# Kernel tuning notes

Hardware: AMD Instinct MI355X
Metric: run time of the kernel (lower is better)

Reference implementation:

```python
import jax, jax.numpy as jnp
import numpy as np
import math

D_MODEL = 1024
NHEAD = 16
FACTOR = 5


def setup_inputs() -> dict:
    key = jax.random.key(0)
    kq, kk, kv = jax.random.split(key, 3)
    B, L = 4, 2048
    Q = jax.random.normal(kq, (B, L, D_MODEL), dtype=jnp.float32)
    K = jax.random.normal(kk, (B, L, D_MODEL), dtype=jnp.float32)
    V = jax.random.normal(kv, (B, L, D_MODEL), dtype=jnp.float32)
    return {"Q": Q, "K": K, "V": V}


def reference(Q, K, V):
    B, q_len, _ = Q.shape
    k_len = K.shape[1]
    head_dim = D_MODEL // NHEAD
    scale = 1.0 / math.sqrt(head_dim)

    # [B, H, L, Dh]
    Qh = Q.reshape(B, q_len, NHEAD, head_dim).transpose(0, 2, 1, 3)
    Kh = K.reshape(B, k_len, NHEAD, head_dim).transpose(0, 2, 1, 3)
    Vh = V.reshape(B, k_len, NHEAD, head_dim).transpose(0, 2, 1, 3)

    # Dense scores for KL-based query selection
    scores = jnp.einsum('bhqd,bhkd->bhqk', Qh, Kh) * scale
    logp = jax.nn.log_softmax(scores, axis=-1)
    probs = jnp.exp(logp)
    # KL(p || uniform) = sum p * (log p + log k_len)
    kl_div = jnp.sum(probs * (logp + jnp.log(jnp.float32(k_len))), axis=-1)  # [B,H,Q]

    top_u = min(int(FACTOR * math.log(q_len)), q_len)
    _, indices = jax.lax.top_k(kl_div, top_u)  # [B,H,U]

    # Gather selected queries
    Q_sparse = jnp.take_along_axis(Qh, indices[..., None], axis=2)  # [B,H,U,Dh]
    scores_sparse = jnp.einsum('bhud,bhkd->bhuk', Q_sparse, Kh) * scale
    attn_weights = jax.nn.softmax(scores_sparse, axis=-1)  # dropout p=0 (eval)
    output_sparse = jnp.einsum('bhuk,bhkd->bhud', attn_weights, Vh)

    # Scatter back into full-length output (non-selected queries are zero)
    b_idx = jnp.arange(B)[:, None, None]
    h_idx = jnp.arange(NHEAD)[None, :, None]
    output_full = jnp.zeros_like(Qh).at[b_idx, h_idx, indices].set(output_sparse)

    output = output_full.transpose(0, 2, 1, 3).reshape(B, q_len, D_MODEL)
    return output, attn_weights
```

## Files before the change

### kernel.cpp

```cpp
#include <hip/hip_runtime.h>
#include <math.h>

#define LQ 2048
#define DM 1024
#define NH 16
#define DH 64
#define UU 38
#define NBH 64
#define SCALE 0.125f

typedef _Float16 f16x8 __attribute__((ext_vector_type(8)));
typedef float f32x4 __attribute__((ext_vector_type(4)));

#if __has_builtin(__builtin_amdgcn_exp2f)
#define EXP2F(x) __builtin_amdgcn_exp2f(x)
#else
#define EXP2F(x) exp2f(x)
#endif

#define F_OFF_SEL   4194304
#define F_OFF_L3    4204032
#define F_OFF_MASK  4213760
#define F_OFF_LPART 4344832
#define F_OFF_KSP   7146496
#define F_NEED      40700928ull

__global__ __launch_bounds__(256) void ksplit_kernel(const float* __restrict__ K,
                                                     _Float16* __restrict__ ksp) {
  int idx = blockIdx.x * 256 + threadIdx.x;
  int p = idx & 7;
  int k = (idx >> 3) & 63;
  int kc = (idx >> 9) & 31;
  int bh = idx >> 14;
  int b = bh >> 4, h = bh & 15;
  const float* src = K + ((size_t)(b * LQ + kc * 64 + k)) * DM + h * DH + (p ^ (k & 7)) * 8;
  float4 x0 = *(const float4*)src;
  float4 x1 = *(const float4*)(src + 4);
  f16x8 hi, lo;
#define KCV(i, xx) { float x_ = (xx); _Float16 hh = (_Float16)x_; hi[i] = hh; lo[i] = (_Float16)(x_ - (float)hh); }
  KCV(0, x0.x) KCV(1, x0.y) KCV(2, x0.z) KCV(3, x0.w)
  KCV(4, x1.x) KCV(5, x1.y) KCV(6, x1.z) KCV(7, x1.w)
#undef KCV
  _Float16* base = ksp + ((size_t)(bh * 32 + kc)) * 8192;
  *(f16x8*)(base + k * 64 + p * 8) = hi;
  *(f16x8*)(base + 4096 + k * 64 + p * 8) = lo;
}

__global__ __launch_bounds__(256) void kl_mfma2(const float* __restrict__ Q,
                                                const _Float16* __restrict__ ksp,
                                                double* __restrict__ lt) {
  int bh = blockIdx.x & 63;
  int qc = (blockIdx.x >> 6) & 15;
  int sp = blockIdx.x >> 10;
  int b = bh >> 4, h = bh & 15;
  int t = threadIdx.x;
  int lane = t & 63, w = t >> 6;
  int quad = lane >> 4, l15 = lane & 15;

  __shared__ __align__(16) _Float16 kbuf[8192];

  f16x8 ahi[2][2], alo[2][2];
  {
    const float* qrow = Q + ((size_t)(b * LQ + qc * 128)) * DM + h * DH;
#pragma unroll
    for (int qt = 0; qt < 2; ++qt)
#pragma unroll
      for (int c = 0; c < 2; ++c) {
        const float* p = qrow + (size_t)(w * 32 + qt * 16 + l15) * DM + c * 32 + quad * 8;
        float4 x0 = *(const float4*)p;
        float4 x1 = *(const float4*)(p + 4);
        f16x8 hi, lo;
#define QCV(i, xx) { float x_ = (xx); _Float16 hh = (_Float16)x_; hi[i] = hh; lo[i] = (_Float16)(x_ - (float)hh); }
        QCV(0, x0.x) QCV(1, x0.y) QCV(2, x0.z) QCV(3, x0.w)
        QCV(4, x1.x) QCV(5, x1.y) QCV(6, x1.z) QCV(7, x1.w)
#undef QCV
        ahi[qt][c] = hi;
        alo[qt][c] = lo;
      }
  }

  int bsw0 = quad ^ (l15 & 7);
  int bsw1 = (quad + 4) ^ (l15 & 7);
  _Float16* khi = kbuf;
  _Float16* klo = kbuf + 4096;
  const float C1 = 0.18033688011112042f;

  double l64[2][4], t64[2][4];
#pragma unroll
  for (int qt = 0; qt < 2; ++qt)
#pragma unroll
    for (int r = 0; r < 4; ++r) { l64[qt][r] = 0.0; t64[qt][r] = 0.0; }

  const uint4* gbase = (const uint4*)(ksp + ((size_t)(bh * 32 + sp * 16)) * 8192);
  uint4* lbuf = (uint4*)kbuf;

  for (int c = 0; c < 16; ++c) {
    const uint4* gsrc = gbase + (size_t)c * 1024;
    __syncthreads();
#pragma unroll
    for (int i = 0; i < 4; ++i) lbuf[i * 256 + t] = gsrc[i * 256 + t];
    __syncthreads();

    float l32[2][4], t32[2][4];
#pragma unroll
    for (int qt = 0; qt < 2; ++qt)
#pragma unroll
      for (int r = 0; r < 4; ++r) { l32[qt][r] = 0.f; t32[qt][r] = 0.f; }

#pragma unroll
    for (int kt = 0; kt < 4; ++kt) {
      int key = kt * 16 + l15;
      f16x8 bhi0 = *(const f16x8*)(khi + key * 64 + bsw0 * 8);
      f16x8 bhi1 = *(const f16x8*)(khi + key * 64 + bsw1 * 8);
      f16x8 blo0 = *(const f16x8*)(klo + key * 64 + bsw0 * 8);
      f16x8 blo1 = *(const f16x8*)(klo + key * 64 + bsw1 * 8);
#pragma unroll
      for (int qt = 0; qt < 2; ++qt) {
        f32x4 cacc = {0.f, 0.f, 0.f, 0.f};
        cacc = __builtin_amdgcn_mfma_f32_16x16x32_f16(alo[qt][0], bhi0, cacc, 0, 0, 0);
        cacc = __builtin_amdgcn_mfma_f32_16x16x32_f16(alo[qt][1], bhi1, cacc, 0, 0, 0);
        cacc = __builtin_amdgcn_mfma_f32_16x16x32_f16(ahi[qt][0], blo0, cacc, 0, 0, 0);
        cacc = __builtin_amdgcn_mfma_f32_16x16x32_f16(ahi[qt][1], blo1, cacc, 0, 0, 0);
        cacc = __builtin_amdgcn_mfma_f32_16x16x32_f16(ahi[qt][0], bhi0, cacc, 0, 0, 0);
        cacc = __builtin_amdgcn_mfma_f32_16x16x32_f16(ahi[qt][1], bhi1, cacc, 0, 0, 0);
#pragma unroll
        for (int r = 0; r < 4; ++r) {
          float rr = cacc[r];
          float e = EXP2F(rr * C1);
          l32[qt][r] += e;
          t32[qt][r] = fmaf(rr, e, t32[qt][r]);
        }
      }
    }
#pragma unroll
    for (int qt = 0; qt < 2; ++qt)
#pragma unroll
      for (int r = 0; r < 4; ++r) {
        l64[qt][r] += (double)l32[qt][r];
        t64[qt][r] += (double)t32[qt][r];
      }
  }

#pragma unroll
  for (int qt = 0; qt < 2; ++qt)
#pragma unroll
    for (int r = 0; r < 4; ++r) {
      double lv = l64[qt][r], tv = t64[qt][r];
#pragma unroll
      for (int m = 1; m < 16; m <<= 1) {
        lv += __shfl_xor(lv, m);
        tv += __shfl_xor(tv, m);
      }
      if (l15 == 0) {
        int qg = qc * 128 + w * 32 + qt * 16 + quad * 4 + r;
        double* dst = lt + ((size_t)(sp * 64 + bh) * LQ + qg) * 2;
        dst[0] = lv;
        dst[1] = tv;
      }
    }
}

__global__ __launch_bounds__(64) void topk2(const double* __restrict__ lt,
                                            int* __restrict__ idxout,
                                            signed char* __restrict__ selmask) {
  int bh = blockIdx.x;
  int lane = threadIdx.x;
  __shared__ double vals[LQ];
  const double logL = 7.624618986159398;
  double bv = -INFINITY;
  int bi = LQ;
  for (int j = 0; j < 32; ++j) {
    int i = j * 64 + lane;
    const double* p0 = lt + ((size_t)bh * LQ + i) * 2;
    const double* p1 = lt + ((size_t)(64 + bh) * LQ + i) * 2;
    double l = p0[0] + p1[0];
    double tt = p0[1] + p1[1];
    double v = 0.125 * (tt / l) - log(l) + logL;
    vals[i] = v;
    selmask[bh * LQ + i] = -1;
    if (v > bv) { bv = v; bi = i; }
  }
  for (int u = 0; u < UU; ++u) {
    double gv = bv;
    int gi = bi;
#pragma unroll
    for (int m = 1; m < 64; m <<= 1) {
      double ov = __shfl_xor(gv, m);
      int oi = __shfl_xor(gi, m);
      if (ov > gv || (ov == gv && oi < gi)) { gv = ov; gi = oi; }
    }
    if (lane == 0) {
      idxout[bh * UU + u] = gi;
      selmask[bh * LQ + gi] = (signed char)u;
    }
    if ((gi & 63) == lane) {
      vals[gi] = -INFINITY;
      bv = -INFINITY;
      bi = LQ;
      for (int j = 0; j < 32; ++j) {
        int i = j * 64 + lane;
        double v = vals[i];
        if (v > bv) { bv = v; bi = i; }
      }
    }
  }
}

__global__ __launch_bounds__(256) void attn_w_mfma(const float* __restrict__ Q,
                                                   const _Float16* __restrict__ ksp,
                                                   const int* __restrict__ sel,
                                                   float* __restrict__ wout,
                                                   float* __restrict__ lpart) {
  int bh = blockIdx.x >> 4;
  int ks = blockIdx.x & 15;
  int b = bh >> 4, h = bh & 15;
  int t = threadIdx.x;
  int lane = t & 63, w = t >> 6;
  int quad = lane >> 4, l15 = lane & 15;

  __shared__ __align__(16) _Float16 kbuf[8192];
  __shared__ float els[48 * 132];
  __shared__ int sidx[UU];

  if (t < UU) sidx[t] = sel[bh * UU + t];
  __syncthreads();

  f16x8 ahi[3][2], alo[3][2];
#pragma unroll
  for (int qt = 0; qt < 3; ++qt) {
    int u = qt * 16 + l15;
    if (u > 37) u = 37;
    const float* qrow = Q + ((size_t)(b * LQ + sidx[u])) * DM + h * DH;
#pragma unroll
    for (int c = 0; c < 2; ++c) {
      const float* p = qrow + c * 32 + quad * 8;
      float4 x0 = *(const float4*)p;
      float4 x1 = *(const float4*)(p + 4);
      f16x8 hi, lo;
#define QCV(i, xx) { float x_ = (xx); _Float16 hh = (_Float16)x_; hi[i] = hh; lo[i] = (_Float16)(x_ - (float)hh); }
      QCV(0, x0.x) QCV(1, x0.y) QCV(2, x0.z) QCV(3, x0.w)
      QCV(4, x1.x) QCV(5, x1.y) QCV(6, x1.z) QCV(7, x1.w)
#undef QCV
      ahi[qt][c] = hi;
      alo[qt][c] = lo;
    }
  }

  int bsw0 = quad ^ (l15 & 7);
  int bsw1 = (quad + 4) ^ (l15 & 7);
  const float C1 = 0.18033688011112042f;
  const uint4* gbase = (const uint4*)(ksp + ((size_t)(bh * 32 + ks * 2)) * 8192);
  uint4* lbuf = (uint4*)kbuf;
  _Float16* khi = kbuf;
  _Float16* klo = kbuf + 4096;

  for (int chunk = 0; chunk < 2; ++chunk) {
    __syncthreads();
#pragma unroll
    for (int i = 0; i < 4; ++i) lbuf[i * 256 + t] = gbase[chunk * 1024 + i * 256 + t];
    __syncthreads();
    int key = w * 16 + l15;
    f16x8 bhi0 = *(const f16x8*)(khi + key * 64 + bsw0 * 8);
    f16x8 bhi1 = *(const f16x8*)(khi + key * 64 + bsw1 * 8);
    f16x8 blo0 = *(const f16x8*)(klo + key * 64 + bsw0 * 8);
    f16x8 blo1 = *(const f16x8*)(klo + key * 64 + bsw1 * 8);
#pragma unroll
    for (int qt = 0; qt < 3; ++qt) {
      f32x4 cacc = {0.f, 0.f, 0.f, 0.f};
      cacc = __builtin_amdgcn_mfma_f32_16x16x32_f16(alo[qt][0], bhi0, cacc, 0, 0, 0);
      cacc = __builtin_amdgcn_mfma_f32_16x16x32_f16(alo[qt][1], bhi1, cacc, 0, 0, 0);
      cacc = __builtin_amdgcn_mfma_f32_16x16x32_f16(ahi[qt][0], blo0, cacc, 0, 0, 0);
      cacc = __builtin_amdgcn_mfma_f32_16x16x32_f16(ahi[qt][1], blo1, cacc, 0, 0, 0);
      cacc = __builtin_amdgcn_mfma_f32_16x16x32_f16(ahi[qt][0], bhi0, cacc, 0, 0, 0);
      cacc = __builtin_amdgcn_mfma_f32_16x16x32_f16(ahi[qt][1], bhi1, cacc, 0, 0, 0);
#pragma unroll
      for (int r = 0; r < 4; ++r) {
        float e = EXP2F(cacc[r] * C1);
        els[(qt * 16 + quad * 4 + r) * 132 + chunk * 64 + w * 16 + l15] = e;
      }
    }
  }
  __syncthreads();

  for (int i = t; i < UU * 128; i += 256) {
    int u = i >> 7, k = i & 127;
    wout[((size_t)(bh * UU + u)) * LQ + ks * 128 + k] = els[u * 132 + k];
  }

#pragma unroll
  for (int p = 0; p < 10; ++p) {
    int u = w + 4 * p;
    if (u < UU) {
      float s = els[u * 132 + lane] + els[u * 132 + 64 + lane];
#pragma unroll
      for (int m = 1; m < 64; m <<= 1) s += __shfl_xor(s, m);
      if (lane == 0) lpart[(bh * 16 + ks) * UU + u] = s;
    }
  }
}

__global__ __launch_bounds__(256) void attn_pv2(const float* __restrict__ V,
                                                const float* __restrict__ wout,
                                                const float* __restrict__ lpart,
                                                float* __restrict__ opart,
                                                float* __restrict__ l3) {
  int bh = blockIdx.x >> 4;
  int ks = blockIdx.x & 15;
  int b = bh >> 4, h = bh & 15;
  int t = threadIdx.x;
  int d = t & 63, ug = t >> 6;

  if (ks == 0 && t < UU) {
    float s = 0.f;
#pragma unroll
    for (int i = 0; i < 16; ++i) s += lpart[(bh * 16 + i) * UU + t];
    l3[bh * UU + t] = s;
  }

  __shared__ float ps[40 * 132];
  for (int i = t; i < UU * 32; i += 256) {
    int u = i >> 5, d4 = i & 31;
    *(float4*)(ps + u * 132 + d4 * 4) =
        *(const float4*)(wout + ((size_t)(bh * UU + u)) * LQ + ks * 128 + d4 * 4);
  }
  for (int i = t; i < 2 * 132; i += 256) ps[UU * 132 + i] = 0.f;
  __syncthreads();

  const float* vbase = V + ((size_t)(b * LQ + ks * 128)) * DM + h * DH + d;
  float o[10];
#pragma unroll
  for (int p = 0; p < 10; ++p) o[p] = 0.f;

  for (int j4 = 0; j4 < 128; j4 += 4) {
    float v0 = vbase[(size_t)(j4 + 0) * DM];
    float v1 = vbase[(size_t)(j4 + 1) * DM];
    float v2 = vbase[(size_t)(j4 + 2) * DM];
    float v3 = vbase[(size_t)(j4 + 3) * DM];
#pragma unroll
    for (int p = 0; p < 10; ++p) {
      float4 pw = *(const float4*)(ps + (ug + 4 * p) * 132 + j4);
      o[p] = fmaf(pw.x, v0, o[p]);
      o[p] = fmaf(pw.y, v1, o[p]);
      o[p] = fmaf(pw.z, v2, o[p]);
      o[p] = fmaf(pw.w, v3, o[p]);
    }
  }

#pragma unroll
  for (int p = 0; p < 10; ++p) {
    int u = ug + 4 * p;
    if (u < UU) opart[((size_t)((bh * 16 + ks) * UU + u)) * DH + d] = o[p];
  }
}

__global__ __launch_bounds__(256) void writeout_kernel(const signed char* __restrict__ selmask,
                                                       const float* __restrict__ l3,
                                                       const float* __restrict__ opart,
                                                       float* __restrict__ out,
                                                       float* __restrict__ wout) {
  const int N1 = NBH * UU * LQ;
  int i = blockIdx.x * 256 + threadIdx.x;
  if (i < N1) {
    wout[i] = wout[i] / l3[i >> 11];
  } else {
    int i2 = i - N1;
    int d = i2 & 63;
    int h = (i2 >> 6) & 15;
    int q = (i2 >> 10) & 2047;
    int b = i2 >> 21;
    int bh = b * 16 + h;
    int u = selmask[bh * LQ + q];
    float val = 0.f;
    if (u >= 0) {
      float s = 0.f;
#pragma unroll
      for (int p = 0; p < 16; ++p)
        s += opart[((size_t)((bh * 16 + p) * UU + u)) * DH + d];
      val = s / l3[bh * UU + u];
    }
    out[i2] = val;
  }
}

extern "C" void kernel_launch(void* const* d_in, const int* in_sizes, int n_in,
                              void* d_out, int out_size, void* d_ws, size_t ws_size,
                              hipStream_t stream) {
  (void)in_sizes; (void)n_in;
  if (ws_size < F_NEED) return;
  const float* Q = (const float*)d_in[0];
  const float* K = (const float*)d_in[1];
  const float* V = (const float*)d_in[2];
  float* out = (float*)d_out;
  float* wout = out + (size_t)4 * LQ * DM;
  char* ws = (char*)d_ws;

  double* lt = (double*)ws;
  int* sel = (int*)(ws + F_OFF_SEL);
  float* l3 = (float*)(ws + F_OFF_L3);
  signed char* mask = (signed char*)(ws + F_OFF_MASK);
  float* lpart = (float*)(ws + F_OFF_LPART);
  _Float16* ksp = (_Float16*)(ws + F_OFF_KSP);
  float* opart = (float*)(ws + F_OFF_KSP);

  ksplit_kernel<<<4096, 256, 0, stream>>>(K, ksp);
  kl_mfma2<<<2048, 256, 0, stream>>>(Q, ksp, lt);
  topk2<<<NBH, 64, 0, stream>>>(lt, sel, mask);
  attn_w_mfma<<<NBH * 16, 256, 0, stream>>>(Q, ksp, sel, wout, lpart);
  attn_pv2<<<NBH * 16, 256, 0, stream>>>(V, wout, lpart, opart, l3);
  writeout_kernel<<<(NBH * UU * LQ + 4 * LQ * DM) / 256, 256, 0, stream>>>(
      mask, l3, opart, out, wout);
}
```

Baseline: 358.9 us.

## Use direct global-to-LDS loads, fuse softmax normalization into PV kernel

K-chunk staging in the KL and attention-weight kernels now uses global_load_lds, copying 16-byte pieces from global memory straight into shared memory instead of going through registers. The KL kernel also promotes its float partial sums to double every two chunks instead of every chunk. The softmax normalization of the attention weights moves into attn_pv2: each block computes the reciprocal row sums, rescales the weights it already loads, and writes them back, so the writeout kernel no longer makes a separate pass over the weights. This removes one read-modify-write pass and some register traffic, at the cost of slightly different float accumulation and redundant row-sum computation in every block.

Result: no change. 359.1 us (+0.1%).

```diff
diff --git a/kernel.cpp b/kernel.cpp
--- a/kernel.cpp
+++ b/kernel.cpp
@@ -17,6 +17,11 @@
 #else
 #define EXP2F(x) exp2f(x)
 #endif
+
+#define GL2LDS16(gp, lp)                                           \
+  __builtin_amdgcn_global_load_lds(                                \
+      (const __attribute__((address_space(1))) void*)(gp),         \
+      (__attribute__((address_space(3))) void*)(lp), 16, 0, 0)
 
 #define F_OFF_SEL   4194304
 #define F_OFF_L3    4204032
@@ -91,21 +96,25 @@
 #pragma unroll
     for (int r = 0; r < 4; ++r) { l64[qt][r] = 0.0; t64[qt][r] = 0.0; }
 
-  const uint4* gbase = (const uint4*)(ksp + ((size_t)(bh * 32 + sp * 16)) * 8192);
-  uint4* lbuf = (uint4*)kbuf;
+  const char* gch = (const char*)(ksp + ((size_t)(bh * 32 + sp * 16)) * 8192);
+  char* lch = (char*)kbuf;
+
+  float l32[2][4], t32[2][4];
+#pragma unroll
+  for (int qt = 0; qt < 2; ++qt)
+#pragma unroll
+    for (int r = 0; r < 4; ++r) { l32[qt][r] = 0.f; t32[qt][r] = 0.f; }
 
   for (int c = 0; c < 16; ++c) {
-    const uint4* gsrc = gbase + (size_t)c * 1024;
     __syncthreads();
-#pragma unroll
-    for (int i = 0; i < 4; ++i) lbuf[i * 256 + t] = gsrc[i * 256 + t];
+    {
+      const char* gs = gch + (size_t)c * 16384 + (size_t)t * 16;
+      char* ls = lch + (size_t)(w * 64) * 16;
+#pragma unroll
+      for (int i = 0; i < 4; ++i)
+        GL2LDS16(gs + i * 4096, ls + i * 4096);
+    }
     __syncthreads();
-
-    float l32[2][4], t32[2][4];
-#pragma unroll
-    for (int qt = 0; qt < 2; ++qt)
-#pragma unroll
-      for (int r = 0; r < 4; ++r) { l32[qt][r] = 0.f; t32[qt][r] = 0.f; }
 
 #pragma unroll
     for (int kt = 0; kt < 4; ++kt) {
@@ -132,13 +141,18 @@
         }
       }
     }
-#pragma unroll
-    for (int qt = 0; qt < 2; ++qt)
-#pragma unroll
-      for (int r = 0; r < 4; ++r) {
-        l64[qt][r] += (double)l32[qt][r];
-        t64[qt][r] += (double)t32[qt][r];
-      }
+
+    if (c & 1) {
+#pragma unroll
+      for (int qt = 0; qt < 2; ++qt)
+#pragma unroll
+        for (int r = 0; r < 4; ++r) {
+          l64[qt][r] += (double)l32[qt][r];
+          t64[qt][r] += (double)t32[qt][r];
+          l32[qt][r] = 0.f;
+          t32[qt][r] = 0.f;
+        }
+    }
   }
 
 #pragma unroll
@@ -249,15 +263,19 @@
   int bsw0 = quad ^ (l15 & 7);
   int bsw1 = (quad + 4) ^ (l15 & 7);
   const float C1 = 0.18033688011112042f;
-  const uint4* gbase = (const uint4*)(ksp + ((size_t)(bh * 32 + ks * 2)) * 8192);
-  uint4* lbuf = (uint4*)kbuf;
+  const char* gch = (const char*)(ksp + ((size_t)(bh * 32 + ks * 2)) * 8192);
   _Float16* khi = kbuf;
   _Float16* klo = kbuf + 4096;
 
   for (int chunk = 0; chunk < 2; ++chunk) {
     __syncthreads();
-#pragma unroll
-    for (int i = 0; i < 4; ++i) lbuf[i * 256 + t] = gbase[chunk * 1024 + i * 256 + t];
+    {
+      const char* gs = gch + (size_t)chunk * 16384 + (size_t)t * 16;
+      char* ls = (char*)kbuf + (size_t)(w * 64) * 16;
+#pragma unroll
+      for (int i = 0; i < 4; ++i)
+        GL2LDS16(gs + i * 4096, ls + i * 4096);
+    }
     __syncthreads();
     int key = w * 16 + l15;
     f16x8 bhi0 = *(const f16x8*)(khi + key * 64 + bsw0 * 8);
@@ -300,30 +318,36 @@
 }
 
 __global__ __launch_bounds__(256) void attn_pv2(const float* __restrict__ V,
-                                                const float* __restrict__ wout,
+                                                float* __restrict__ wout,
                                                 const float* __restrict__ lpart,
-                                                float* __restrict__ opart,
-                                                float* __restrict__ l3) {
+                                                float* __restrict__ opart) {
   int bh = blockIdx.x >> 4;
   int ks = blockIdx.x & 15;
   int b = bh >> 4, h = bh & 15;
   int t = threadIdx.x;
   int d = t & 63, ug = t >> 6;
 
-  if (ks == 0 && t < UU) {
+  __shared__ float ps[40 * 132];
+  __shared__ float l3s[UU];
+
+  if (t < UU) {
     float s = 0.f;
 #pragma unroll
     for (int i = 0; i < 16; ++i) s += lpart[(bh * 16 + i) * UU + t];
-    l3[bh * UU + t] = s;
-  }
-
-  __shared__ float ps[40 * 132];
+    l3s[t] = 1.f / s;
+  }
+  for (int i = t; i < 2 * 132; i += 256) ps[UU * 132 + i] = 0.f;
+  __syncthreads();
+
   for (int i = t; i < UU * 32; i += 256) {
     int u = i >> 5, d4 = i & 31;
-    *(float4*)(ps + u * 132 + d4 * 4) =
-        *(const float4*)(wout + ((size_t)(bh * UU + u)) * LQ + ks * 128 + d4 * 4);
-  }
-  for (int i = t; i < 2 * 132; i += 256) ps[UU * 132 + i] = 0.f;
+    float r = l3s[u];
+    float* wp = wout + ((size_t)(bh * UU + u)) * LQ + ks * 128 + d4 * 4;
+    float4 v = *(const float4*)wp;
+    v.x *= r; v.y *= r; v.z *= r; v.w *= r;
+    *(float4*)(ps + u * 132 + d4 * 4) = v;
+    *(float4*)wp = v;
+  }
   __syncthreads();
 
   const float* vbase = V + ((size_t)(b * LQ + ks * 128)) * DM + h * DH + d;
@@ -354,32 +378,24 @@
 }
 
 __global__ __launch_bounds__(256) void writeout_kernel(const signed char* __restrict__ selmask,
-                                                       const float* __restrict__ l3,
                                                        const float* __restrict__ opart,
-                                                       float* __restrict__ out,
-                                                       float* __restrict__ wout) {
-  const int N1 = NBH * UU * LQ;
-  int i = blockIdx.x * 256 + threadIdx.x;
-  if (i < N1) {
-    wout[i] = wout[i] / l3[i >> 11];
-  } else {
-    int i2 = i - N1;
-    int d = i2 & 63;
-    int h = (i2 >> 6) & 15;
-    int q = (i2 >> 10) & 2047;
-    int b = i2 >> 21;
-    int bh = b * 16 + h;
-    int u = selmask[bh * LQ + q];
-    float val = 0.f;
-    if (u >= 0) {
-      float s = 0.f;
-#pragma unroll
-      for (int p = 0; p < 16; ++p)
-        s += opart[((size_t)((bh * 16 + p) * UU + u)) * DH + d];
-      val = s / l3[bh * UU + u];
-    }
-    out[i2] = val;
-  }
+                                                       float* __restrict__ out) {
+  int i2 = blockIdx.x * 256 + threadIdx.x;
+  int d = i2 & 63;
+  int h = (i2 >> 6) & 15;
+  int q = (i2 >> 10) & 2047;
+  int b = i2 >> 21;
+  int bh = b * 16 + h;
+  int u = selmask[bh * LQ + q];
+  float val = 0.f;
+  if (u >= 0) {
+    float s = 0.f;
+#pragma unroll
+    for (int p = 0; p < 16; ++p)
+      s += opart[((size_t)((bh * 16 + p) * UU + u)) * DH + d];
+    val = s;
+  }
+  out[i2] = val;
 }
 
 extern "C" void kernel_launch(void* const* d_in, const int* in_sizes, int n_in,
@@ -396,7 +412,6 @@
 
   double* lt = (double*)ws;
   int* sel = (int*)(ws + F_OFF_SEL);
-  float* l3 = (float*)(ws + F_OFF_L3);
   signed char* mask = (signed char*)(ws + F_OFF_MASK);
   float* lpart = (float*)(ws + F_OFF_LPART);
   _Float16* ksp = (_Float16*)(ws + F_OFF_KSP);
@@ -406,7 +421,6 @@
   kl_mfma2<<<2048, 256, 0, stream>>>(Q, ksp, lt);
   topk2<<<NBH, 64, 0, stream>>>(lt, sel, mask);
   attn_w_mfma<<<NBH * 16, 256, 0, stream>>>(Q, ksp, sel, wout, lpart);
-  attn_pv2<<<NBH * 16, 256, 0, stream>>>(V, wout, lpart, opart, l3);
-  writeout_kernel<<<(NBH * UU * LQ + 4 * LQ * DM) / 256, 256, 0, stream>>>(
-      mask, l3, opart, out, wout);
-}
+  attn_pv2<<<NBH * 16, 256, 0, stream>>>(V, wout, lpart, opart);
+  writeout_kernel<<<(4 * LQ * DM) / 256, 256, 0, stream>>>(mask, opart, out);
+}
```
